# Optimization experiments

Measured on AMD Instinct MI355X. Metric: run time of the kernel, lower is better.

Reference implementation:

```python
import jax, jax.numpy as jnp
import numpy as np

N_NODES = 50000
N_EDGES = 600000
HID = 128
N_CONVS = 3
N_GRAPHS = 64


def setup_inputs() -> dict:
    key = jax.random.key(0)
    ks = jax.random.split(key, 8)
    scale = 1.0 / np.sqrt(HID)  # ~xavier
    node_attr = jax.random.normal(ks[0], (N_NODES, HID), dtype=jnp.float32)
    edge_attr = jax.random.normal(ks[1], (N_EDGES, HID), dtype=jnp.float32)
    edge_index = jax.random.randint(ks[2], (2, N_EDGES), 0, N_NODES, dtype=jnp.int32)
    batch = jnp.sort(jax.random.randint(ks[3], (N_NODES,), 0, N_GRAPHS, dtype=jnp.int32))
    W1 = jax.random.normal(ks[4], (N_CONVS, HID, HID), dtype=jnp.float32) * scale
    B1 = jnp.zeros((N_CONVS, HID), dtype=jnp.float32)
    W2 = jax.random.normal(ks[5], (N_CONVS, HID, HID), dtype=jnp.float32) * scale
    B2 = jnp.zeros((N_CONVS, HID), dtype=jnp.float32)
    return {"node_attr": node_attr, "edge_attr": edge_attr, "edge_index": edge_index,
            "batch": batch, "W1": W1, "B1": B1, "W2": W2, "B2": B2,
            "num_graphs": N_GRAPHS}


def _gine_conv(x, edge_index, edge_attr, w1, b1, w2, b2, eps=0.0):
    src, dst = edge_index[0], edge_index[1]
    # message: softplus(x_j + edge_attr), gathered from source nodes
    msg = jax.nn.softplus(x[src] + edge_attr)          # [E, H]
    agg = jax.ops.segment_sum(msg, dst, num_segments=x.shape[0])  # [N, H]
    out = agg + (1.0 + eps) * x
    # MLP: Linear -> softplus -> Linear (torch Linear: y = x @ W.T + b)
    h = jax.nn.softplus(out @ w1.T + b1)
    return h @ w2.T + b2


def reference(node_attr, edge_attr, edge_index, batch, W1, B1, W2, B2, num_graphs):
    x = node_attr
    for i in range(N_CONVS):
        h = _gine_conv(x, edge_index, edge_attr, W1[i], B1[i], W2[i], B2[i])
        if i < N_CONVS - 1:
            h = jax.nn.softplus(h)  # inter-layer activation
        x = h
    node_feature = x
    graph_feature = jax.ops.segment_sum(node_feature, batch, num_segments=num_graphs)
    return graph_feature, node_feature
```

## Files before the change

kernel.cpp:

```cpp
#include <hip/hip_runtime.h>
#include <math.h>

#define N_NODES 50000
#define N_EDGES 600000
#define HID 128
#define N_GRAPHS 64
#define BCAP 32
#define OVF_CAP 4096
#define PCHUNK 8
#define LDSP 136

typedef __attribute__((ext_vector_type(8))) short short8;
typedef __attribute__((ext_vector_type(4))) float floatx4;

__device__ __forceinline__ float softplus_f(float v) {
    return fmaxf(v, 0.0f) + __logf(1.0f + __expf(-fabsf(v)));
}
__device__ __forceinline__ unsigned short f2bf(float f) {
    unsigned u = __float_as_uint(f);
    u = (u + 0x7FFFu + ((u >> 16) & 1u)) >> 16;
    return (unsigned short)u;
}
__device__ __forceinline__ float bflo(unsigned u) { return __uint_as_float(u << 16); }
__device__ __forceinline__ float bfhi(unsigned u) { return __uint_as_float(u & 0xFFFF0000u); }

__global__ void pack_x(const float* __restrict__ xf, unsigned short* __restrict__ xb, int nelem4) {
    int t = blockIdx.x * 256 + threadIdx.x;
    if (t >= nelem4) return;
    float4 v = *(const float4*)(xf + (size_t)t * 4);
    unsigned o0 = (unsigned)f2bf(v.x) | ((unsigned)f2bf(v.y) << 16);
    unsigned o1 = (unsigned)f2bf(v.z) | ((unsigned)f2bf(v.w) << 16);
    *(uint2*)(xb + (size_t)t * 4) = make_uint2(o0, o1);
}

__global__ void build_buckets(const int* __restrict__ ei, int* __restrict__ cnt,
                              int2* __restrict__ bkt, int4* __restrict__ ovf) {
    int e = blockIdx.x * 256 + threadIdx.x;
    if (e >= N_EDGES) return;
    int src = ei[e];
    int dst = ei[N_EDGES + e];
    int slot = atomicAdd(&cnt[dst], 1);
    if (slot < BCAP) {
        bkt[(size_t)dst * BCAP + slot] = make_int2(e, src);
    } else {
        int k = atomicAdd(&cnt[N_NODES], 1);
        if (k < OVF_CAP) ovf[k] = make_int4(e, src, dst, 0);
    }
}

__global__ void __launch_bounds__(256) agg_kernel(const unsigned short* __restrict__ xb,
        const float* __restrict__ edge_attr, const int* __restrict__ cnt,
        const int2* __restrict__ bkt, const int4* __restrict__ ovf,
        unsigned short* __restrict__ outb) {
    int wave = blockIdx.x * 4 + (threadIdx.x >> 6);
    int lane = threadIdx.x & 63;
    int n = __builtin_amdgcn_readfirstlane(wave);
    if (n >= N_NODES) return;
    int h = lane >> 5;
    int l = lane & 31;
    int ctot = cnt[n];
    int c = ctot < BCAP ? ctot : BCAP;
    const int2* bk = bkt + (size_t)n * BCAP;
    float4 acc = make_float4(0.f, 0.f, 0.f, 0.f);
    int s = 0;
    for (; s + 4 <= c; s += 4) {
        int2 pA = bk[s + h];
        int2 pB = bk[s + 2 + h];
        float4 eA = *(const float4*)(edge_attr + (size_t)pA.x * HID + l * 4);
        uint2  xA = *(const uint2*)(xb + (size_t)pA.y * HID + l * 4);
        float4 eB = *(const float4*)(edge_attr + (size_t)pB.x * HID + l * 4);
        uint2  xB = *(const uint2*)(xb + (size_t)pB.y * HID + l * 4);
        acc.x += softplus_f(eA.x + bflo(xA.x)) + softplus_f(eB.x + bflo(xB.x));
        acc.y += softplus_f(eA.y + bfhi(xA.x)) + softplus_f(eB.y + bfhi(xB.x));
        acc.z += softplus_f(eA.z + bflo(xA.y)) + softplus_f(eB.z + bflo(xB.y));
        acc.w += softplus_f(eA.w + bfhi(xA.y)) + softplus_f(eB.w + bfhi(xB.y));
    }
    if (s + 2 <= c) {
        int2 p = bk[s + h];
        float4 ev = *(const float4*)(edge_attr + (size_t)p.x * HID + l * 4);
        uint2  xv = *(const uint2*)(xb + (size_t)p.y * HID + l * 4);
        acc.x += softplus_f(ev.x + bflo(xv.x));
        acc.y += softplus_f(ev.y + bfhi(xv.x));
        acc.z += softplus_f(ev.z + bflo(xv.y));
        acc.w += softplus_f(ev.w + bfhi(xv.y));
        s += 2;
    }
    if (s < c && h == 0) {
        int2 p = bk[s];
        float4 ev = *(const float4*)(edge_attr + (size_t)p.x * HID + l * 4);
        uint2  xv = *(const uint2*)(xb + (size_t)p.y * HID + l * 4);
        acc.x += softplus_f(ev.x + bflo(xv.x));
        acc.y += softplus_f(ev.y + bfhi(xv.x));
        acc.z += softplus_f(ev.z + bflo(xv.y));
        acc.w += softplus_f(ev.w + bfhi(xv.y));
    }
    if (ctot > BCAP) {
        int k = cnt[N_NODES]; if (k > OVF_CAP) k = OVF_CAP;
        for (int i = 0; i < k; i++) {
            int4 t = ovf[i];
            if (t.z == n && h == 0) {
                float4 ev = *(const float4*)(edge_attr + (size_t)t.x * HID + l * 4);
                uint2  xv = *(const uint2*)(xb + (size_t)t.y * HID + l * 4);
                acc.x += softplus_f(ev.x + bflo(xv.x));
                acc.y += softplus_f(ev.y + bfhi(xv.x));
                acc.z += softplus_f(ev.z + bflo(xv.y));
                acc.w += softplus_f(ev.w + bfhi(xv.y));
            }
        }
    }
    acc.x += __shfl(acc.x, l + 32);
    acc.y += __shfl(acc.y, l + 32);
    acc.z += __shfl(acc.z, l + 32);
    acc.w += __shfl(acc.w, l + 32);
    if (h == 0) {
        uint2 xn = *(const uint2*)(xb + (size_t)n * HID + l * 4);
        acc.x += bflo(xn.x); acc.y += bfhi(xn.x);
        acc.z += bflo(xn.y); acc.w += bfhi(xn.y);
        unsigned o0 = (unsigned)f2bf(acc.x) | ((unsigned)f2bf(acc.y) << 16);
        unsigned o1 = (unsigned)f2bf(acc.z) | ((unsigned)f2bf(acc.w) << 16);
        *(uint2*)(outb + (size_t)n * HID + l * 4) = make_uint2(o0, o1);
    }
}

__global__ void pack_w(const float* __restrict__ W1, const float* __restrict__ W2,
                       unsigned short* __restrict__ pw) {
    int t = blockIdx.x * 256 + threadIdx.x;
    if (t >= 6 * 32 * 64) return;
    int lane = t & 63;
    int tile = (t >> 6) & 31;
    int mat = t >> 11;
    int kt = tile >> 3, nt = tile & 7;
    const float* W = (mat & 1) ? W2 : W1;
    W += (size_t)(mat >> 1) * HID * HID;
    int n = nt * 16 + (lane & 15);
    int kbase = kt * 32 + (lane >> 4) * 8;
    short8 v;
    #pragma unroll
    for (int j = 0; j < 8; j++) v[j] = (short)f2bf(W[(size_t)n * HID + kbase + j]);
    *((short8*)(pw + (size_t)t * 8)) = v;
}

__global__ void __launch_bounds__(256) mlp_fused(const unsigned short* __restrict__ A,
        const unsigned short* __restrict__ pw1, const unsigned short* __restrict__ pw2,
        const float* __restrict__ b1, const float* __restrict__ b2,
        void* __restrict__ outp, int final_layer) {
    __shared__ __align__(16) unsigned short hl[2][16][LDSP];
    int wave = threadIdx.x >> 6, lane = threadIdx.x & 63;
    int rt = wave >> 1, ch = wave & 1;
    int m = lane & 15, q = lane >> 4;
    int r0 = blockIdx.x * 32 + rt * 16;
    int row = r0 + m;
    bool rv = row < N_NODES;
    short8 zf = {0, 0, 0, 0, 0, 0, 0, 0};
    floatx4 zero = {0.f, 0.f, 0.f, 0.f};
    floatx4 acc[4];
    #pragma unroll
    for (int t = 0; t < 4; t++) acc[t] = zero;
    const short8* ar = (const short8*)(A + (size_t)row * HID + q * 8);
    const short8* w1 = (const short8*)pw1;
    #pragma unroll
    for (int kt = 0; kt < 4; kt++) {
        short8 af = rv ? ar[kt * 4] : zf;
        const short8* wp = w1 + (size_t)(kt * 8 + ch * 4) * 64 + lane;
        #pragma unroll
        for (int t = 0; t < 4; t++)
            acc[t] = __builtin_amdgcn_mfma_f32_16x16x32_bf16(af, wp[t * 64], acc[t], 0, 0, 0);
    }
    #pragma unroll
    for (int t = 0; t < 4; t++) {
        int col = ch * 64 + t * 16 + m;
        float bb = b1[col];
        #pragma unroll
        for (int i = 0; i < 4; i++)
            hl[rt][q * 4 + i][col] = f2bf(softplus_f(acc[t][i] + bb));
    }
    __syncthreads();
    #pragma unroll
    for (int t = 0; t < 4; t++) acc[t] = zero;
    const short8* w2 = (const short8*)pw2;
    #pragma unroll
    for (int kt = 0; kt < 4; kt++) {
        short8 af = *(const short8*)&hl[rt][m][kt * 32 + q * 8];
        const short8* wp = w2 + (size_t)(kt * 8 + ch * 4) * 64 + lane;
        #pragma unroll
        for (int t = 0; t < 4; t++)
            acc[t] = __builtin_amdgcn_mfma_f32_16x16x32_bf16(af, wp[t * 64], acc[t], 0, 0, 0);
    }
    if (final_layer) {
        float* out = (float*)outp;
        #pragma unroll
        for (int t = 0; t < 4; t++) {
            int col = ch * 64 + t * 16 + m;
            float bb = b2[col];
            #pragma unroll
            for (int i = 0; i < 4; i++) {
                int r = r0 + q * 4 + i;
                if (r < N_NODES) out[(size_t)r * HID + col] = acc[t][i] + bb;
            }
        }
    } else {
        __syncthreads();
        #pragma unroll
        for (int t = 0; t < 4; t++) {
            int col = ch * 64 + t * 16 + m;
            float bb = b2[col];
            #pragma unroll
            for (int i = 0; i < 4; i++)
                hl[rt][q * 4 + i][col] = f2bf(softplus_f(acc[t][i] + bb));
        }
        __syncthreads();
        unsigned short* outb = (unsigned short*)outp;
        int tid = threadIdx.x;
        int orow = tid >> 3, cseg = (tid & 7) * 16;
        int gr = blockIdx.x * 32 + orow;
        if (gr < N_NODES) {
            uint4 v0 = *(const uint4*)&hl[orow >> 4][orow & 15][cseg];
            uint4 v1 = *(const uint4*)&hl[orow >> 4][orow & 15][cseg + 8];
            *(uint4*)(outb + (size_t)gr * HID + cseg) = v0;
            *(uint4*)(outb + (size_t)gr * HID + cseg + 8) = v1;
        }
    }
}

__global__ void find_bounds(const int* __restrict__ batch, int* __restrict__ start) {
    int n = blockIdx.x * 256 + threadIdx.x;
    if (n >= N_NODES) return;
    int bn = batch[n];
    int bp = (n == 0) ? -1 : batch[n - 1];
    for (int g = bp + 1; g <= bn; g++) start[g] = n;
    if (n == N_NODES - 1)
        for (int g = bn + 1; g <= N_GRAPHS; g++) start[g] = N_NODES;
}

__global__ void pool_partial(const float* __restrict__ nf, const int* __restrict__ start,
                             float* __restrict__ part) {
    int g = blockIdx.x >> 3, c = blockIdx.x & (PCHUNK - 1);
    int j = threadIdx.x;
    int s = start[g], e = start[g + 1];
    int len = e - s;
    int b0 = s + (len * c) / PCHUNK;
    int b1 = s + (len * (c + 1)) / PCHUNK;
    float acc = 0.f;
    for (int n = b0; n < b1; n++) acc += nf[(size_t)n * HID + j];
    part[(size_t)blockIdx.x * HID + j] = acc;
}

__global__ void pool_final(const float* __restrict__ part, float* __restrict__ gout) {
    int g = blockIdx.x, j = threadIdx.x;
    float acc = 0.f;
    #pragma unroll
    for (int c = 0; c < PCHUNK; c++) acc += part[(size_t)(g * PCHUNK + c) * HID + j];
    gout[(size_t)g * HID + j] = acc;
}

extern "C" void kernel_launch(void* const* d_in, const int* in_sizes, int n_in,
                              void* d_out, int out_size, void* d_ws, size_t ws_size,
                              hipStream_t stream) {
    const float* node_attr = (const float*)d_in[0];
    const float* edge_attr = (const float*)d_in[1];
    const int*   ei        = (const int*)d_in[2];
    const int*   batch     = (const int*)d_in[3];
    const float* W1        = (const float*)d_in[4];
    const float* B1        = (const float*)d_in[5];
    const float* W2        = (const float*)d_in[6];
    const float* B2        = (const float*)d_in[7];

    float* gout    = (float*)d_out;
    float* nodeout = (float*)d_out + N_GRAPHS * HID;

    const size_t NH = (size_t)N_NODES * HID;
    unsigned short* nab  = (unsigned short*)d_ws;
    unsigned short* bufA = nab + NH;
    unsigned short* bufB = bufA + NH;
    int*   cnt = (int*)(bufB + NH);
    int4*  ovf = (int4*)(cnt + 50004);
    int2*  bkt = (int2*)(ovf + OVF_CAP);
    unsigned short* pw = (unsigned short*)(bkt + (size_t)N_NODES * BCAP);
    int*   startb = (int*)(pw + 6 * 16384);
    float* part = (float*)(startb + 68);

    hipMemsetAsync(cnt, 0, (size_t)50001 * sizeof(int), stream);
    build_buckets<<<(N_EDGES + 255) / 256, 256, 0, stream>>>(ei, cnt, bkt, ovf);
    pack_w<<<(6 * 32 * 64 + 255) / 256, 256, 0, stream>>>(W1, W2, pw);
    pack_x<<<((int)(NH / 4) + 255) / 256, 256, 0, stream>>>(node_attr, nab, (int)(NH / 4));
    find_bounds<<<(N_NODES + 255) / 256, 256, 0, stream>>>(batch, startb);

    const int agg_blocks = (N_NODES + 3) / 4;
    const int mlp_blocks = (N_NODES + 31) / 32;

    const unsigned short* xcur = nab;
    for (int i = 0; i < 3; i++) {
        agg_kernel<<<agg_blocks, 256, 0, stream>>>(xcur, edge_attr, cnt, bkt, ovf, bufA);
        void* outp = (i == 2) ? (void*)nodeout : (void*)bufB;
        mlp_fused<<<mlp_blocks, 256, 0, stream>>>(bufA,
                pw + (size_t)(i * 2) * 16384, pw + (size_t)(i * 2 + 1) * 16384,
                B1 + (size_t)i * HID, B2 + (size_t)i * HID, outp, (i == 2) ? 1 : 0);
        xcur = bufB;
    }
    pool_partial<<<N_GRAPHS * PCHUNK, HID, 0, stream>>>(nodeout, startb, part);
    pool_final<<<N_GRAPHS, HID, 0, stream>>>(part, gout);
}
```

Before: 746.5 us.

## Cache edge_attr as bf16 during first aggregation and reuse it in later layers

The first-layer aggregation now writes a bf16 copy of edge_attr while it reads the fp32 values. The second and third layers read that half-size copy instead of fp32. Each lane now handles 8 features, so 4 edges are processed per wave step instead of 2, with an xor-shuffle reduction across the quarter-waves. This cuts the edge_attr traffic that dominates the later layers, at the cost of extra writes in layer one, bf16 rounding of edge features, and a larger workspace.

Result: slower. 777.0 us (+4.1%).

```diff
diff --git a/kernel.cpp b/kernel.cpp
--- a/kernel.cpp
+++ b/kernel.cpp
@@ -48,77 +48,129 @@
     }
 }
 
-__global__ void __launch_bounds__(256) agg_kernel(const unsigned short* __restrict__ xb,
-        const float* __restrict__ edge_attr, const int* __restrict__ cnt,
-        const int2* __restrict__ bkt, const int4* __restrict__ ovf,
-        unsigned short* __restrict__ outb) {
+__device__ __forceinline__ void acc8_bf(float* acc, uint4 ev, uint4 xv) {
+    acc[0] += softplus_f(bflo(ev.x) + bflo(xv.x));
+    acc[1] += softplus_f(bfhi(ev.x) + bfhi(xv.x));
+    acc[2] += softplus_f(bflo(ev.y) + bflo(xv.y));
+    acc[3] += softplus_f(bfhi(ev.y) + bfhi(xv.y));
+    acc[4] += softplus_f(bflo(ev.z) + bflo(xv.z));
+    acc[5] += softplus_f(bfhi(ev.z) + bfhi(xv.z));
+    acc[6] += softplus_f(bflo(ev.w) + bflo(xv.w));
+    acc[7] += softplus_f(bfhi(ev.w) + bfhi(xv.w));
+}
+__device__ __forceinline__ void acc8_f32(float* acc, float4 e0, float4 e1, uint4 xv) {
+    acc[0] += softplus_f(e0.x + bflo(xv.x));
+    acc[1] += softplus_f(e0.y + bfhi(xv.x));
+    acc[2] += softplus_f(e0.z + bflo(xv.y));
+    acc[3] += softplus_f(e0.w + bfhi(xv.y));
+    acc[4] += softplus_f(e1.x + bflo(xv.z));
+    acc[5] += softplus_f(e1.y + bfhi(xv.z));
+    acc[6] += softplus_f(e1.z + bflo(xv.w));
+    acc[7] += softplus_f(e1.w + bfhi(xv.w));
+}
+__device__ __forceinline__ void store_bf8(unsigned short* __restrict__ eb, int e, int l,
+                                          float4 e0, float4 e1) {
+    uint4 st;
+    st.x = (unsigned)f2bf(e0.x) | ((unsigned)f2bf(e0.y) << 16);
+    st.y = (unsigned)f2bf(e0.z) | ((unsigned)f2bf(e0.w) << 16);
+    st.z = (unsigned)f2bf(e1.x) | ((unsigned)f2bf(e1.y) << 16);
+    st.w = (unsigned)f2bf(e1.z) | ((unsigned)f2bf(e1.w) << 16);
+    *(uint4*)(eb + (size_t)e * HID + l * 8) = st;
+}
+
+template<int L0>
+__global__ void __launch_bounds__(256) agg_kernel_t(const unsigned short* __restrict__ xb,
+        const float* __restrict__ ef, unsigned short* __restrict__ eb,
+        const int* __restrict__ cnt, const int2* __restrict__ bkt,
+        const int4* __restrict__ ovf, unsigned short* __restrict__ outb) {
     int wave = blockIdx.x * 4 + (threadIdx.x >> 6);
     int lane = threadIdx.x & 63;
     int n = __builtin_amdgcn_readfirstlane(wave);
     if (n >= N_NODES) return;
-    int h = lane >> 5;
-    int l = lane & 31;
+    int q = lane >> 4;
+    int l = lane & 15;
     int ctot = cnt[n];
     int c = ctot < BCAP ? ctot : BCAP;
     const int2* bk = bkt + (size_t)n * BCAP;
-    float4 acc = make_float4(0.f, 0.f, 0.f, 0.f);
+    float acc[8];
+    #pragma unroll
+    for (int j = 0; j < 8; j++) acc[j] = 0.f;
     int s = 0;
-    for (; s + 4 <= c; s += 4) {
-        int2 pA = bk[s + h];
-        int2 pB = bk[s + 2 + h];
-        float4 eA = *(const float4*)(edge_attr + (size_t)pA.x * HID + l * 4);
-        uint2  xA = *(const uint2*)(xb + (size_t)pA.y * HID + l * 4);
-        float4 eB = *(const float4*)(edge_attr + (size_t)pB.x * HID + l * 4);
-        uint2  xB = *(const uint2*)(xb + (size_t)pB.y * HID + l * 4);
-        acc.x += softplus_f(eA.x + bflo(xA.x)) + softplus_f(eB.x + bflo(xB.x));
-        acc.y += softplus_f(eA.y + bfhi(xA.x)) + softplus_f(eB.y + bfhi(xB.x));
-        acc.z += softplus_f(eA.z + bflo(xA.y)) + softplus_f(eB.z + bflo(xB.y));
-        acc.w += softplus_f(eA.w + bfhi(xA.y)) + softplus_f(eB.w + bfhi(xB.y));
-    }
-    if (s + 2 <= c) {
-        int2 p = bk[s + h];
-        float4 ev = *(const float4*)(edge_attr + (size_t)p.x * HID + l * 4);
-        uint2  xv = *(const uint2*)(xb + (size_t)p.y * HID + l * 4);
-        acc.x += softplus_f(ev.x + bflo(xv.x));
-        acc.y += softplus_f(ev.y + bfhi(xv.x));
-        acc.z += softplus_f(ev.z + bflo(xv.y));
-        acc.w += softplus_f(ev.w + bfhi(xv.y));
-        s += 2;
-    }
-    if (s < c && h == 0) {
-        int2 p = bk[s];
-        float4 ev = *(const float4*)(edge_attr + (size_t)p.x * HID + l * 4);
-        uint2  xv = *(const uint2*)(xb + (size_t)p.y * HID + l * 4);
-        acc.x += softplus_f(ev.x + bflo(xv.x));
-        acc.y += softplus_f(ev.y + bfhi(xv.x));
-        acc.z += softplus_f(ev.z + bflo(xv.y));
-        acc.w += softplus_f(ev.w + bfhi(xv.y));
+    for (; s + 8 <= c; s += 8) {
+        int2 pA = bk[s + q];
+        int2 pB = bk[s + 4 + q];
+        if (L0) {
+            float4 a0 = *(const float4*)(ef + (size_t)pA.x * HID + l * 8);
+            float4 a1 = *(const float4*)(ef + (size_t)pA.x * HID + l * 8 + 4);
+            uint4  xa = *(const uint4*)(xb + (size_t)pA.y * HID + l * 8);
+            float4 b0 = *(const float4*)(ef + (size_t)pB.x * HID + l * 8);
+            float4 b1 = *(const float4*)(ef + (size_t)pB.x * HID + l * 8 + 4);
+            uint4  xv = *(const uint4*)(xb + (size_t)pB.y * HID + l * 8);
+            store_bf8(eb, pA.x, l, a0, a1);
+            store_bf8(eb, pB.x, l, b0, b1);
+            acc8_f32(acc, a0, a1, xa);
+            acc8_f32(acc, b0, b1, xv);
+        } else {
+            uint4 ea = *(const uint4*)(eb + (size_t)pA.x * HID + l * 8);
+            uint4 xa = *(const uint4*)(xb + (size_t)pA.y * HID + l * 8);
+            uint4 ec = *(const uint4*)(eb + (size_t)pB.x * HID + l * 8);
+            uint4 xv = *(const uint4*)(xb + (size_t)pB.y * HID + l * 8);
+            acc8_bf(acc, ea, xa);
+            acc8_bf(acc, ec, xv);
+        }
+    }
+    for (; s < c; s += 4) {
+        if (s + q < c) {
+            int2 p = bk[s + q];
+            if (L0) {
+                float4 e0 = *(const float4*)(ef + (size_t)p.x * HID + l * 8);
+                float4 e1 = *(const float4*)(ef + (size_t)p.x * HID + l * 8 + 4);
+                uint4  xv = *(const uint4*)(xb + (size_t)p.y * HID + l * 8);
+                store_bf8(eb, p.x, l, e0, e1);
+                acc8_f32(acc, e0, e1, xv);
+            } else {
+                uint4 ev = *(const uint4*)(eb + (size_t)p.x * HID + l * 8);
+                uint4 xv = *(const uint4*)(xb + (size_t)p.y * HID + l * 8);
+                acc8_bf(acc, ev, xv);
+            }
+        }
     }
     if (ctot > BCAP) {
         int k = cnt[N_NODES]; if (k > OVF_CAP) k = OVF_CAP;
         for (int i = 0; i < k; i++) {
             int4 t = ovf[i];
-            if (t.z == n && h == 0) {
-                float4 ev = *(const float4*)(edge_attr + (size_t)t.x * HID + l * 4);
-                uint2  xv = *(const uint2*)(xb + (size_t)t.y * HID + l * 4);
-                acc.x += softplus_f(ev.x + bflo(xv.x));
-                acc.y += softplus_f(ev.y + bfhi(xv.x));
-                acc.z += softplus_f(ev.z + bflo(xv.y));
-                acc.w += softplus_f(ev.w + bfhi(xv.y));
+            if (t.z == n && q == 0) {
+                if (L0) {
+                    float4 e0 = *(const float4*)(ef + (size_t)t.x * HID + l * 8);
+                    float4 e1 = *(const float4*)(ef + (size_t)t.x * HID + l * 8 + 4);
+                    uint4  xv = *(const uint4*)(xb + (size_t)t.y * HID + l * 8);
+                    store_bf8(eb, t.x, l, e0, e1);
+                    acc8_f32(acc, e0, e1, xv);
+                } else {
+                    uint4 ev = *(const uint4*)(eb + (size_t)t.x * HID + l * 8);
+                    uint4 xv = *(const uint4*)(xb + (size_t)t.y * HID + l * 8);
+                    acc8_bf(acc, ev, xv);
+                }
             }
         }
     }
-    acc.x += __shfl(acc.x, l + 32);
-    acc.y += __shfl(acc.y, l + 32);
-    acc.z += __shfl(acc.z, l + 32);
-    acc.w += __shfl(acc.w, l + 32);
-    if (h == 0) {
-        uint2 xn = *(const uint2*)(xb + (size_t)n * HID + l * 4);
-        acc.x += bflo(xn.x); acc.y += bfhi(xn.x);
-        acc.z += bflo(xn.y); acc.w += bfhi(xn.y);
-        unsigned o0 = (unsigned)f2bf(acc.x) | ((unsigned)f2bf(acc.y) << 16);
-        unsigned o1 = (unsigned)f2bf(acc.z) | ((unsigned)f2bf(acc.w) << 16);
-        *(uint2*)(outb + (size_t)n * HID + l * 4) = make_uint2(o0, o1);
+    #pragma unroll
+    for (int j = 0; j < 8; j++) {
+        acc[j] += __shfl_xor(acc[j], 16);
+        acc[j] += __shfl_xor(acc[j], 32);
+    }
+    if (q == 0) {
+        uint4 xn = *(const uint4*)(xb + (size_t)n * HID + l * 8);
+        acc[0] += bflo(xn.x); acc[1] += bfhi(xn.x);
+        acc[2] += bflo(xn.y); acc[3] += bfhi(xn.y);
+        acc[4] += bflo(xn.z); acc[5] += bfhi(xn.z);
+        acc[6] += bflo(xn.w); acc[7] += bfhi(xn.w);
+        uint4 o;
+        o.x = (unsigned)f2bf(acc[0]) | ((unsigned)f2bf(acc[1]) << 16);
+        o.y = (unsigned)f2bf(acc[2]) | ((unsigned)f2bf(acc[3]) << 16);
+        o.z = (unsigned)f2bf(acc[4]) | ((unsigned)f2bf(acc[5]) << 16);
+        o.w = (unsigned)f2bf(acc[6]) | ((unsigned)f2bf(acc[7]) << 16);
+        *(uint4*)(outb + (size_t)n * HID + l * 8) = o;
     }
 }
 
@@ -278,6 +330,7 @@
     unsigned short* pw = (unsigned short*)(bkt + (size_t)N_NODES * BCAP);
     int*   startb = (int*)(pw + 6 * 16384);
     float* part = (float*)(startb + 68);
+    unsigned short* eb = (unsigned short*)(part + (size_t)N_GRAPHS * PCHUNK * HID);
 
     hipMemsetAsync(cnt, 0, (size_t)50001 * sizeof(int), stream);
     build_buckets<<<(N_EDGES + 255) / 256, 256, 0, stream>>>(ei, cnt, bkt, ovf);
@@ -290,7 +343,10 @@
 
     const unsigned short* xcur = nab;
     for (int i = 0; i < 3; i++) {
-        agg_kernel<<<agg_blocks, 256, 0, stream>>>(xcur, edge_attr, cnt, bkt, ovf, bufA);
+        if (i == 0)
+            agg_kernel_t<1><<<agg_blocks, 256, 0, stream>>>(xcur, edge_attr, eb, cnt, bkt, ovf, bufA);
+        else
+            agg_kernel_t<0><<<agg_blocks, 256, 0, stream>>>(xcur, edge_attr, eb, cnt, bkt, ovf, bufA);
         void* outp = (i == 2) ? (void*)nodeout : (void*)bufB;
         mlp_fused<<<mlp_blocks, 256, 0, stream>>>(bufA,
                 pw + (size_t)(i * 2) * 16384, pw + (size_t)(i * 2 + 1) * 16384,
```

## Fuse edge aggregation into MLP kernel using LDS atomic accumulation per node tile

Applied to the files above, without the earlier changes.

Merges the per-node aggregation kernel and the MLP kernel into a single per-layer kernel. Each block takes 32 nodes, flattens their bucketed edges into an LDS work list, gathers edge and source features with a software-prefetched pipeline, and accumulates softplus messages into LDS with float atomics. The result is converted to bf16 in registers and fed straight to the MFMA MLP, which removes the global round trip of the aggregated tensor and one launch per layer. In exchange it adds LDS atomic contention and several block-wide syncs, and the block-parallel edge loop replaces the one-wave-per-node design.

New measurement: 1.783 ms. 139% more time.

```diff
diff --git a/kernel.cpp b/kernel.cpp
--- a/kernel.cpp
+++ b/kernel.cpp
@@ -9,6 +9,8 @@
 #define OVF_CAP 4096
 #define PCHUNK 8
 #define LDSP 136
+#define NB 32
+#define AST 132
 
 typedef __attribute__((ext_vector_type(8))) short short8;
 typedef __attribute__((ext_vector_type(4))) float floatx4;
@@ -45,80 +47,6 @@
     } else {
         int k = atomicAdd(&cnt[N_NODES], 1);
         if (k < OVF_CAP) ovf[k] = make_int4(e, src, dst, 0);
-    }
-}
-
-__global__ void __launch_bounds__(256) agg_kernel(const unsigned short* __restrict__ xb,
-        const float* __restrict__ edge_attr, const int* __restrict__ cnt,
-        const int2* __restrict__ bkt, const int4* __restrict__ ovf,
-        unsigned short* __restrict__ outb) {
-    int wave = blockIdx.x * 4 + (threadIdx.x >> 6);
-    int lane = threadIdx.x & 63;
-    int n = __builtin_amdgcn_readfirstlane(wave);
-    if (n >= N_NODES) return;
-    int h = lane >> 5;
-    int l = lane & 31;
-    int ctot = cnt[n];
-    int c = ctot < BCAP ? ctot : BCAP;
-    const int2* bk = bkt + (size_t)n * BCAP;
-    float4 acc = make_float4(0.f, 0.f, 0.f, 0.f);
-    int s = 0;
-    for (; s + 4 <= c; s += 4) {
-        int2 pA = bk[s + h];
-        int2 pB = bk[s + 2 + h];
-        float4 eA = *(const float4*)(edge_attr + (size_t)pA.x * HID + l * 4);
-        uint2  xA = *(const uint2*)(xb + (size_t)pA.y * HID + l * 4);
-        float4 eB = *(const float4*)(edge_attr + (size_t)pB.x * HID + l * 4);
-        uint2  xB = *(const uint2*)(xb + (size_t)pB.y * HID + l * 4);
-        acc.x += softplus_f(eA.x + bflo(xA.x)) + softplus_f(eB.x + bflo(xB.x));
-        acc.y += softplus_f(eA.y + bfhi(xA.x)) + softplus_f(eB.y + bfhi(xB.x));
-        acc.z += softplus_f(eA.z + bflo(xA.y)) + softplus_f(eB.z + bflo(xB.y));
-        acc.w += softplus_f(eA.w + bfhi(xA.y)) + softplus_f(eB.w + bfhi(xB.y));
-    }
-    if (s + 2 <= c) {
-        int2 p = bk[s + h];
-        float4 ev = *(const float4*)(edge_attr + (size_t)p.x * HID + l * 4);
-        uint2  xv = *(const uint2*)(xb + (size_t)p.y * HID + l * 4);
-        acc.x += softplus_f(ev.x + bflo(xv.x));
-        acc.y += softplus_f(ev.y + bfhi(xv.x));
-        acc.z += softplus_f(ev.z + bflo(xv.y));
-        acc.w += softplus_f(ev.w + bfhi(xv.y));
-        s += 2;
-    }
-    if (s < c && h == 0) {
-        int2 p = bk[s];
-        float4 ev = *(const float4*)(edge_attr + (size_t)p.x * HID + l * 4);
-        uint2  xv = *(const uint2*)(xb + (size_t)p.y * HID + l * 4);
-        acc.x += softplus_f(ev.x + bflo(xv.x));
-        acc.y += softplus_f(ev.y + bfhi(xv.x));
-        acc.z += softplus_f(ev.z + bflo(xv.y));
-        acc.w += softplus_f(ev.w + bfhi(xv.y));
-    }
-    if (ctot > BCAP) {
-        int k = cnt[N_NODES]; if (k > OVF_CAP) k = OVF_CAP;
-        for (int i = 0; i < k; i++) {
-            int4 t = ovf[i];
-            if (t.z == n && h == 0) {
-                float4 ev = *(const float4*)(edge_attr + (size_t)t.x * HID + l * 4);
-                uint2  xv = *(const uint2*)(xb + (size_t)t.y * HID + l * 4);
-                acc.x += softplus_f(ev.x + bflo(xv.x));
-                acc.y += softplus_f(ev.y + bfhi(xv.x));
-                acc.z += softplus_f(ev.z + bflo(xv.y));
-                acc.w += softplus_f(ev.w + bfhi(xv.y));
-            }
-        }
-    }
-    acc.x += __shfl(acc.x, l + 32);
-    acc.y += __shfl(acc.y, l + 32);
-    acc.z += __shfl(acc.z, l + 32);
-    acc.w += __shfl(acc.w, l + 32);
-    if (h == 0) {
-        uint2 xn = *(const uint2*)(xb + (size_t)n * HID + l * 4);
-        acc.x += bflo(xn.x); acc.y += bfhi(xn.x);
-        acc.z += bflo(xn.y); acc.w += bfhi(xn.y);
-        unsigned o0 = (unsigned)f2bf(acc.x) | ((unsigned)f2bf(acc.y) << 16);
-        unsigned o1 = (unsigned)f2bf(acc.z) | ((unsigned)f2bf(acc.w) << 16);
-        *(uint2*)(outb + (size_t)n * HID + l * 4) = make_uint2(o0, o1);
     }
 }
 
@@ -140,31 +68,138 @@
     *((short8*)(pw + (size_t)t * 8)) = v;
 }
 
-__global__ void __launch_bounds__(256) mlp_fused(const unsigned short* __restrict__ A,
+__global__ void __launch_bounds__(256) layer_fused(
+        const unsigned short* __restrict__ xb,
+        const float* __restrict__ ef,
+        const int* __restrict__ cnt, const int2* __restrict__ bkt,
+        const int4* __restrict__ ovf,
         const unsigned short* __restrict__ pw1, const unsigned short* __restrict__ pw2,
         const float* __restrict__ b1, const float* __restrict__ b2,
         void* __restrict__ outp, int final_layer) {
-    __shared__ __align__(16) unsigned short hl[2][16][LDSP];
-    int wave = threadIdx.x >> 6, lane = threadIdx.x & 63;
+    __shared__ __align__(16) char smem[19216];
+    float* accf = (float*)smem;
+    unsigned short* s_list = (unsigned short*)(smem + 16896);
+    int* s_cnt  = (int*)(smem + 18944);
+    int* s_off  = (int*)(smem + 19072);
+    int* s_misc = (int*)(smem + 19208);
+
+    int tid = threadIdx.x;
+    int n0 = blockIdx.x * NB;
+
+    for (int i = tid; i < NB * AST; i += 256) accf[i] = 0.f;
+    if (tid < NB) {
+        int n = n0 + tid;
+        s_cnt[tid] = (n < N_NODES) ? cnt[n] : 0;
+    }
+    __syncthreads();
+    if (tid == 0) {
+        int o = 0, ov = 0;
+        #pragma unroll 4
+        for (int i = 0; i < NB; i++) {
+            int cc = s_cnt[i];
+            if (cc > BCAP) { ov = 1; cc = BCAP; }
+            s_off[i] = o; o += cc;
+        }
+        s_off[NB] = o; s_misc[0] = o; s_misc[1] = ov;
+    }
+    __syncthreads();
+    if (tid < NB) {
+        int cc = s_cnt[tid]; if (cc > BCAP) cc = BCAP;
+        int o = s_off[tid];
+        for (int j = 0; j < cc; j++) s_list[o + j] = (unsigned short)((tid << 6) | j);
+    }
+    __syncthreads();
+
+    int tot = s_misc[0];
+    int hw = tid >> 5, l = tid & 31;
+
+    if (tot > 0) {
+        int2 pA, pB;
+        float4 evA; uint2 xvA;
+        {
+            int ka = (hw < tot) ? hw : 0;
+            int va = s_list[ka];
+            pA = bkt[(size_t)(n0 + (va >> 6)) * BCAP + (va & 63)];
+            int kb = (hw + 8 < tot) ? hw + 8 : 0;
+            int vb = s_list[kb];
+            pB = bkt[(size_t)(n0 + (vb >> 6)) * BCAP + (vb & 63)];
+            evA = *(const float4*)(ef + (size_t)pA.x * HID + l * 4);
+            xvA = *(const uint2*)(xb + (size_t)pA.y * HID + l * 4);
+        }
+        for (int k = hw; k < tot; k += 8) {
+            float4 evN = *(const float4*)(ef + (size_t)pB.x * HID + l * 4);
+            uint2  xvN = *(const uint2*)(xb + (size_t)pB.y * HID + l * 4);
+            int kc = (k + 16 < tot) ? k + 16 : 0;
+            int vc = s_list[kc];
+            int2 pN = bkt[(size_t)(n0 + (vc >> 6)) * BCAP + (vc & 63)];
+            int ln = s_list[k] >> 6;
+            float* ac = accf + ln * AST + l * 4;
+            atomicAdd(ac + 0, softplus_f(evA.x + bflo(xvA.x)));
+            atomicAdd(ac + 1, softplus_f(evA.y + bfhi(xvA.x)));
+            atomicAdd(ac + 2, softplus_f(evA.z + bflo(xvA.y)));
+            atomicAdd(ac + 3, softplus_f(evA.w + bfhi(xvA.y)));
+            pB = pN; evA = evN; xvA = xvN;
+        }
+    }
+    if (s_misc[1]) {
+        int kov = cnt[N_NODES]; if (kov > OVF_CAP) kov = OVF_CAP;
+        if (hw == 0) {
+            for (int i = 0; i < kov; i++) {
+                int4 t = ovf[i];
+                if (t.z >= n0 && t.z < n0 + NB) {
+                    float4 ev = *(const float4*)(ef + (size_t)t.x * HID + l * 4);
+                    uint2  xv = *(const uint2*)(xb + (size_t)t.y * HID + l * 4);
+                    float* ac = accf + (t.z - n0) * AST + l * 4;
+                    atomicAdd(ac + 0, softplus_f(ev.x + bflo(xv.x)));
+                    atomicAdd(ac + 1, softplus_f(ev.y + bfhi(xv.x)));
+                    atomicAdd(ac + 2, softplus_f(ev.z + bflo(xv.y)));
+                    atomicAdd(ac + 3, softplus_f(ev.w + bfhi(xv.y)));
+                }
+            }
+        }
+    }
+    __syncthreads();
+
+    int wave = tid >> 6, lane = tid & 63;
     int rt = wave >> 1, ch = wave & 1;
     int m = lane & 15, q = lane >> 4;
-    int r0 = blockIdx.x * 32 + rt * 16;
+    int r0 = n0 + rt * 16;
     int row = r0 + m;
     bool rv = row < N_NODES;
-    short8 zf = {0, 0, 0, 0, 0, 0, 0, 0};
+    int lm = rt * 16 + m;
+
+    short8 af[4];
+    #pragma unroll
+    for (int kt = 0; kt < 4; kt++) {
+        const float* ap = accf + (size_t)lm * AST + kt * 32 + q * 8;
+        float4 a0 = *(const float4*)(ap);
+        float4 a1 = *(const float4*)(ap + 4);
+        uint4 xv = rv ? *(const uint4*)(xb + (size_t)row * HID + kt * 32 + q * 8)
+                      : make_uint4(0, 0, 0, 0);
+        af[kt][0] = (short)f2bf(a0.x + bflo(xv.x));
+        af[kt][1] = (short)f2bf(a0.y + bfhi(xv.x));
+        af[kt][2] = (short)f2bf(a0.z + bflo(xv.y));
+        af[kt][3] = (short)f2bf(a0.w + bfhi(xv.y));
+        af[kt][4] = (short)f2bf(a1.x + bflo(xv.z));
+        af[kt][5] = (short)f2bf(a1.y + bfhi(xv.z));
+        af[kt][6] = (short)f2bf(a1.z + bflo(xv.w));
+        af[kt][7] = (short)f2bf(a1.w + bfhi(xv.w));
+    }
+    __syncthreads();
+
+    unsigned short* hlp = (unsigned short*)smem;
+
     floatx4 zero = {0.f, 0.f, 0.f, 0.f};
     floatx4 acc[4];
     #pragma unroll
     for (int t = 0; t < 4; t++) acc[t] = zero;
-    const short8* ar = (const short8*)(A + (size_t)row * HID + q * 8);
     const short8* w1 = (const short8*)pw1;
     #pragma unroll
     for (int kt = 0; kt < 4; kt++) {
-        short8 af = rv ? ar[kt * 4] : zf;
         const short8* wp = w1 + (size_t)(kt * 8 + ch * 4) * 64 + lane;
         #pragma unroll
         for (int t = 0; t < 4; t++)
-            acc[t] = __builtin_amdgcn_mfma_f32_16x16x32_bf16(af, wp[t * 64], acc[t], 0, 0, 0);
+            acc[t] = __builtin_amdgcn_mfma_f32_16x16x32_bf16(af[kt], wp[t * 64], acc[t], 0, 0, 0);
     }
     #pragma unroll
     for (int t = 0; t < 4; t++) {
@@ -172,7 +207,7 @@
         float bb = b1[col];
         #pragma unroll
         for (int i = 0; i < 4; i++)
-            hl[rt][q * 4 + i][col] = f2bf(softplus_f(acc[t][i] + bb));
+            hlp[(size_t)(rt * 16 + q * 4 + i) * LDSP + col] = f2bf(softplus_f(acc[t][i] + bb));
     }
     __syncthreads();
     #pragma unroll
@@ -180,11 +215,11 @@
     const short8* w2 = (const short8*)pw2;
     #pragma unroll
     for (int kt = 0; kt < 4; kt++) {
-        short8 af = *(const short8*)&hl[rt][m][kt * 32 + q * 8];
+        short8 hf = *(const short8*)&hlp[(size_t)(rt * 16 + m) * LDSP + kt * 32 + q * 8];
         const short8* wp = w2 + (size_t)(kt * 8 + ch * 4) * 64 + lane;
         #pragma unroll
         for (int t = 0; t < 4; t++)
-            acc[t] = __builtin_amdgcn_mfma_f32_16x16x32_bf16(af, wp[t * 64], acc[t], 0, 0, 0);
+            acc[t] = __builtin_amdgcn_mfma_f32_16x16x32_bf16(hf, wp[t * 64], acc[t], 0, 0, 0);
     }
     if (final_layer) {
         float* out = (float*)outp;
@@ -206,16 +241,15 @@
             float bb = b2[col];
             #pragma unroll
             for (int i = 0; i < 4; i++)
-                hl[rt][q * 4 + i][col] = f2bf(softplus_f(acc[t][i] + bb));
+                hlp[(size_t)(rt * 16 + q * 4 + i) * LDSP + col] = f2bf(softplus_f(acc[t][i] + bb));
         }
         __syncthreads();
         unsigned short* outb = (unsigned short*)outp;
-        int tid = threadIdx.x;
         int orow = tid >> 3, cseg = (tid & 7) * 16;
-        int gr = blockIdx.x * 32 + orow;
+        int gr = n0 + orow;
         if (gr < N_NODES) {
-            uint4 v0 = *(const uint4*)&hl[orow >> 4][orow & 15][cseg];
-            uint4 v1 = *(const uint4*)&hl[orow >> 4][orow & 15][cseg + 8];
+            uint4 v0 = *(const uint4*)&hlp[(size_t)orow * LDSP + cseg];
+            uint4 v1 = *(const uint4*)&hlp[(size_t)orow * LDSP + cseg + 8];
             *(uint4*)(outb + (size_t)gr * HID + cseg) = v0;
             *(uint4*)(outb + (size_t)gr * HID + cseg + 8) = v1;
         }
@@ -270,9 +304,9 @@
 
     const size_t NH = (size_t)N_NODES * HID;
     unsigned short* nab  = (unsigned short*)d_ws;
-    unsigned short* bufA = nab + NH;
-    unsigned short* bufB = bufA + NH;
-    int*   cnt = (int*)(bufB + NH);
+    unsigned short* buf0 = nab + NH;
+    unsigned short* buf1 = buf0 + NH;
+    int*   cnt = (int*)(buf1 + NH);
     int4*  ovf = (int4*)(cnt + 50004);
     int2*  bkt = (int2*)(ovf + OVF_CAP);
     unsigned short* pw = (unsigned short*)(bkt + (size_t)N_NODES * BCAP);
@@ -285,17 +319,14 @@
     pack_x<<<((int)(NH / 4) + 255) / 256, 256, 0, stream>>>(node_attr, nab, (int)(NH / 4));
     find_bounds<<<(N_NODES + 255) / 256, 256, 0, stream>>>(batch, startb);
 
-    const int agg_blocks = (N_NODES + 3) / 4;
-    const int mlp_blocks = (N_NODES + 31) / 32;
-
-    const unsigned short* xcur = nab;
+    const int blocks = (N_NODES + NB - 1) / NB;
+
+    const unsigned short* xin[3] = { nab, buf0, buf1 };
+    void* xout[3] = { (void*)buf0, (void*)buf1, (void*)nodeout };
     for (int i = 0; i < 3; i++) {
-        agg_kernel<<<agg_blocks, 256, 0, stream>>>(xcur, edge_attr, cnt, bkt, ovf, bufA);
-        void* outp = (i == 2) ? (void*)nodeout : (void*)bufB;
-        mlp_fused<<<mlp_blocks, 256, 0, stream>>>(bufA,
+        layer_fused<<<blocks, 256, 0, stream>>>(xin[i], edge_attr, cnt, bkt, ovf,
                 pw + (size_t)(i * 2) * 16384, pw + (size_t)(i * 2 + 1) * 16384,
-                B1 + (size_t)i * HID, B2 + (size_t)i * HID, outp, (i == 2) ? 1 : 0);
-        xcur = bufB;
+                B1 + (size_t)i * HID, B2 + (size_t)i * HID, xout[i], (i == 2) ? 1 : 0);
     }
     pool_partial<<<N_GRAPHS * PCHUNK, HID, 0, stream>>>(nodeout, startb, part);
     pool_final<<<N_GRAPHS, HID, 0, stream>>>(part, gout);
```

## Stage edge_attr as bf16 in destination-sorted order for later aggregation passes

Applied to the files above, without the earlier changes.

In the first aggregation pass each node reserves a contiguous slot range with an atomic counter and writes its in-bucket edge features as bf16 into a compacted buffer. Later passes read these contiguous bf16 rows instead of gathering fp32 rows of edge_attr by edge id. This halves edge-feature bytes and turns random gathers into mostly sequential reads, at the cost of an extra write in pass 0 and bf16 rounding of edge_attr. Overflow edges still read the fp32 source.

After: 1.187 ms. 59.0% more time.

```diff
diff --git a/kernel.cpp b/kernel.cpp
--- a/kernel.cpp
+++ b/kernel.cpp
@@ -23,6 +23,12 @@
 }
 __device__ __forceinline__ float bflo(unsigned u) { return __uint_as_float(u << 16); }
 __device__ __forceinline__ float bfhi(unsigned u) { return __uint_as_float(u & 0xFFFF0000u); }
+__device__ __forceinline__ uint2 bfpack4(float4 v) {
+    uint2 o;
+    o.x = (unsigned)f2bf(v.x) | ((unsigned)f2bf(v.y) << 16);
+    o.y = (unsigned)f2bf(v.z) | ((unsigned)f2bf(v.w) << 16);
+    return o;
+}
 
 __global__ void pack_x(const float* __restrict__ xf, unsigned short* __restrict__ xb, int nelem4) {
     int t = blockIdx.x * 256 + threadIdx.x;
@@ -48,10 +54,11 @@
     }
 }
 
-__global__ void __launch_bounds__(256) agg_kernel(const unsigned short* __restrict__ xb,
+__global__ void __launch_bounds__(256) agg_pass0(const unsigned short* __restrict__ xb,
         const float* __restrict__ edge_attr, const int* __restrict__ cnt,
         const int2* __restrict__ bkt, const int4* __restrict__ ovf,
-        unsigned short* __restrict__ outb) {
+        unsigned short* __restrict__ outb,
+        unsigned short* __restrict__ ebs, int* __restrict__ off, int* __restrict__ galloc) {
     int wave = blockIdx.x * 4 + (threadIdx.x >> 6);
     int lane = threadIdx.x & 63;
     int n = __builtin_amdgcn_readfirstlane(wave);
@@ -60,6 +67,12 @@
     int l = lane & 31;
     int ctot = cnt[n];
     int c = ctot < BCAP ? ctot : BCAP;
+    int pos0 = 0;
+    if (lane == 0 && c > 0) {
+        pos0 = atomicAdd(galloc, c);
+        off[n] = pos0;
+    }
+    pos0 = __shfl(pos0, 0);
     const int2* bk = bkt + (size_t)n * BCAP;
     float4 acc = make_float4(0.f, 0.f, 0.f, 0.f);
     int s = 0;
@@ -70,6 +83,8 @@
         uint2  xA = *(const uint2*)(xb + (size_t)pA.y * HID + l * 4);
         float4 eB = *(const float4*)(edge_attr + (size_t)pB.x * HID + l * 4);
         uint2  xB = *(const uint2*)(xb + (size_t)pB.y * HID + l * 4);
+        *(uint2*)(ebs + (size_t)(pos0 + s + h) * HID + l * 4) = bfpack4(eA);
+        *(uint2*)(ebs + (size_t)(pos0 + s + 2 + h) * HID + l * 4) = bfpack4(eB);
         acc.x += softplus_f(eA.x + bflo(xA.x)) + softplus_f(eB.x + bflo(xB.x));
         acc.y += softplus_f(eA.y + bfhi(xA.x)) + softplus_f(eB.y + bfhi(xB.x));
         acc.z += softplus_f(eA.z + bflo(xA.y)) + softplus_f(eB.z + bflo(xB.y));
@@ -79,6 +94,7 @@
         int2 p = bk[s + h];
         float4 ev = *(const float4*)(edge_attr + (size_t)p.x * HID + l * 4);
         uint2  xv = *(const uint2*)(xb + (size_t)p.y * HID + l * 4);
+        *(uint2*)(ebs + (size_t)(pos0 + s + h) * HID + l * 4) = bfpack4(ev);
         acc.x += softplus_f(ev.x + bflo(xv.x));
         acc.y += softplus_f(ev.y + bfhi(xv.x));
         acc.z += softplus_f(ev.z + bflo(xv.y));
@@ -89,10 +105,88 @@
         int2 p = bk[s];
         float4 ev = *(const float4*)(edge_attr + (size_t)p.x * HID + l * 4);
         uint2  xv = *(const uint2*)(xb + (size_t)p.y * HID + l * 4);
+        *(uint2*)(ebs + (size_t)(pos0 + s) * HID + l * 4) = bfpack4(ev);
         acc.x += softplus_f(ev.x + bflo(xv.x));
         acc.y += softplus_f(ev.y + bfhi(xv.x));
         acc.z += softplus_f(ev.z + bflo(xv.y));
         acc.w += softplus_f(ev.w + bfhi(xv.y));
+    }
+    if (ctot > BCAP) {
+        int k = cnt[N_NODES]; if (k > OVF_CAP) k = OVF_CAP;
+        for (int i = 0; i < k; i++) {
+            int4 t = ovf[i];
+            if (t.z == n && h == 0) {
+                float4 ev = *(const float4*)(edge_attr + (size_t)t.x * HID + l * 4);
+                uint2  xv = *(const uint2*)(xb + (size_t)t.y * HID + l * 4);
+                acc.x += softplus_f(ev.x + bflo(xv.x));
+                acc.y += softplus_f(ev.y + bfhi(xv.x));
+                acc.z += softplus_f(ev.z + bflo(xv.y));
+                acc.w += softplus_f(ev.w + bfhi(xv.y));
+            }
+        }
+    }
+    acc.x += __shfl(acc.x, l + 32);
+    acc.y += __shfl(acc.y, l + 32);
+    acc.z += __shfl(acc.z, l + 32);
+    acc.w += __shfl(acc.w, l + 32);
+    if (h == 0) {
+        uint2 xn = *(const uint2*)(xb + (size_t)n * HID + l * 4);
+        acc.x += bflo(xn.x); acc.y += bfhi(xn.x);
+        acc.z += bflo(xn.y); acc.w += bfhi(xn.y);
+        unsigned o0 = (unsigned)f2bf(acc.x) | ((unsigned)f2bf(acc.y) << 16);
+        unsigned o1 = (unsigned)f2bf(acc.z) | ((unsigned)f2bf(acc.w) << 16);
+        *(uint2*)(outb + (size_t)n * HID + l * 4) = make_uint2(o0, o1);
+    }
+}
+
+__global__ void __launch_bounds__(256) agg_pass12(const unsigned short* __restrict__ xb,
+        const float* __restrict__ edge_attr, const int* __restrict__ cnt,
+        const int2* __restrict__ bkt, const int4* __restrict__ ovf,
+        unsigned short* __restrict__ outb,
+        const unsigned short* __restrict__ ebs, const int* __restrict__ off) {
+    int wave = blockIdx.x * 4 + (threadIdx.x >> 6);
+    int lane = threadIdx.x & 63;
+    int n = __builtin_amdgcn_readfirstlane(wave);
+    if (n >= N_NODES) return;
+    int h = lane >> 5;
+    int l = lane & 31;
+    int ctot = cnt[n];
+    int c = ctot < BCAP ? ctot : BCAP;
+    int p0 = (c > 0) ? off[n] : 0;
+    const int2* bk = bkt + (size_t)n * BCAP;
+    const unsigned short* er = ebs + (size_t)p0 * HID;
+    float4 acc = make_float4(0.f, 0.f, 0.f, 0.f);
+    int s = 0;
+    for (; s + 4 <= c; s += 4) {
+        int2 pA = bk[s + h];
+        int2 pB = bk[s + 2 + h];
+        uint2 eA = *(const uint2*)(er + (size_t)(s + h) * HID + l * 4);
+        uint2 xA = *(const uint2*)(xb + (size_t)pA.y * HID + l * 4);
+        uint2 eB = *(const uint2*)(er + (size_t)(s + 2 + h) * HID + l * 4);
+        uint2 xB = *(const uint2*)(xb + (size_t)pB.y * HID + l * 4);
+        acc.x += softplus_f(bflo(eA.x) + bflo(xA.x)) + softplus_f(bflo(eB.x) + bflo(xB.x));
+        acc.y += softplus_f(bfhi(eA.x) + bfhi(xA.x)) + softplus_f(bfhi(eB.x) + bfhi(xB.x));
+        acc.z += softplus_f(bflo(eA.y) + bflo(xA.y)) + softplus_f(bflo(eB.y) + bflo(xB.y));
+        acc.w += softplus_f(bfhi(eA.y) + bfhi(xA.y)) + softplus_f(bfhi(eB.y) + bfhi(xB.y));
+    }
+    if (s + 2 <= c) {
+        int2 p = bk[s + h];
+        uint2 ev = *(const uint2*)(er + (size_t)(s + h) * HID + l * 4);
+        uint2 xv = *(const uint2*)(xb + (size_t)p.y * HID + l * 4);
+        acc.x += softplus_f(bflo(ev.x) + bflo(xv.x));
+        acc.y += softplus_f(bfhi(ev.x) + bfhi(xv.x));
+        acc.z += softplus_f(bflo(ev.y) + bflo(xv.y));
+        acc.w += softplus_f(bfhi(ev.y) + bfhi(xv.y));
+        s += 2;
+    }
+    if (s < c && h == 0) {
+        int2 p = bk[s];
+        uint2 ev = *(const uint2*)(er + (size_t)s * HID + l * 4);
+        uint2 xv = *(const uint2*)(xb + (size_t)p.y * HID + l * 4);
+        acc.x += softplus_f(bflo(ev.x) + bflo(xv.x));
+        acc.y += softplus_f(bfhi(ev.x) + bfhi(xv.x));
+        acc.z += softplus_f(bflo(ev.y) + bflo(xv.y));
+        acc.w += softplus_f(bfhi(ev.y) + bfhi(xv.y));
     }
     if (ctot > BCAP) {
         int k = cnt[N_NODES]; if (k > OVF_CAP) k = OVF_CAP;
@@ -273,13 +367,15 @@
     unsigned short* bufA = nab + NH;
     unsigned short* bufB = bufA + NH;
     int*   cnt = (int*)(bufB + NH);
-    int4*  ovf = (int4*)(cnt + 50004);
+    int4*  ovf = (int4*)(cnt + 50008);
     int2*  bkt = (int2*)(ovf + OVF_CAP);
     unsigned short* pw = (unsigned short*)(bkt + (size_t)N_NODES * BCAP);
     int*   startb = (int*)(pw + 6 * 16384);
     float* part = (float*)(startb + 68);
-
-    hipMemsetAsync(cnt, 0, (size_t)50001 * sizeof(int), stream);
+    int*   off = (int*)(part + (size_t)N_GRAPHS * PCHUNK * HID);
+    unsigned short* ebs = (unsigned short*)(off + 50000);
+
+    hipMemsetAsync(cnt, 0, (size_t)50002 * sizeof(int), stream);
     build_buckets<<<(N_EDGES + 255) / 256, 256, 0, stream>>>(ei, cnt, bkt, ovf);
     pack_w<<<(6 * 32 * 64 + 255) / 256, 256, 0, stream>>>(W1, W2, pw);
     pack_x<<<((int)(NH / 4) + 255) / 256, 256, 0, stream>>>(node_attr, nab, (int)(NH / 4));
@@ -290,7 +386,12 @@
 
     const unsigned short* xcur = nab;
     for (int i = 0; i < 3; i++) {
-        agg_kernel<<<agg_blocks, 256, 0, stream>>>(xcur, edge_attr, cnt, bkt, ovf, bufA);
+        if (i == 0)
+            agg_pass0<<<agg_blocks, 256, 0, stream>>>(xcur, edge_attr, cnt, bkt, ovf,
+                    bufA, ebs, off, cnt + 50001);
+        else
+            agg_pass12<<<agg_blocks, 256, 0, stream>>>(xcur, edge_attr, cnt, bkt, ovf,
+                    bufA, ebs, off);
         void* outp = (i == 2) ? (void*)nodeout : (void*)bufB;
         mlp_fused<<<mlp_blocks, 256, 0, stream>>>(bufA,
                 pw + (size_t)(i * 2) * 16384, pw + (size_t)(i * 2 + 1) * 16384,
```
